# Kernel tuning notes

Hardware: AMD Instinct MI355X
Metric: run time of the kernel (lower is better)

## Reference

```python
import jax, jax.numpy as jnp
import numpy as np

VOCAB, EMBED, CONV_C, HID, LABELS = 50257, 512, 512, 1024, 128
B, S = 32, 1024

def setup_inputs() -> dict:
    key = jax.random.key(0)
    ks = jax.random.split(key, 8)
    sc = lambda d: 1.0 / np.sqrt(d)
    return {
        "token_ids": jax.random.randint(ks[0], (B, S), 0, VOCAB),
        "emb_table": jax.random.normal(ks[1], (VOCAB, EMBED), jnp.float32) * 0.02,
        "conv_w": jax.random.normal(ks[2], (CONV_C, EMBED), jnp.float32) * sc(EMBED),
        "conv_b": jnp.zeros((CONV_C,), jnp.float32),
        "dec_w1": jax.random.normal(ks[3], (CONV_C, HID), jnp.float32) * sc(CONV_C),
        "dec_b1": jnp.zeros((HID,), jnp.float32),
        "dec_w2": jax.random.normal(ks[4], (HID, LABELS), jnp.float32) * sc(HID),
        "dec_b2": jnp.zeros((LABELS,), jnp.float32),
    }

def reference(token_ids, emb_table, conv_w, conv_b, dec_w1, dec_b1, dec_w2, dec_b2):
    # Embedding lookup: [B, S, E]
    x = emb_table[token_ids]
    # DocNN encoder on a length-1 sequence = kernel-1 conv + relu (+ trivial max-over-time)
    h = jax.nn.relu(jnp.einsum('bse,ce->bsc', x, conv_w) + conv_b)  # [B,S,C]
    # MLP decoder per word
    z = jax.nn.relu(jnp.einsum('bsc,ch->bsh', h, dec_w1) + dec_b1)  # [B,S,H]
    logits = jnp.einsum('bsh,hl->bsl', z, dec_w2) + dec_b2          # [B,S,L]
    # torch.cat over dim 0 of per-word outputs -> flat [B*S, L]
    return logits.reshape(-1, logits.shape[-1])
```

## Files before the change

kernel.cpp:

```cpp
#include <hip/hip_runtime.h>

typedef __bf16 bf16;
typedef __bf16 bf16x4 __attribute__((ext_vector_type(4)));
typedef __bf16 bf16x8 __attribute__((ext_vector_type(8)));
typedef float f32x4 __attribute__((ext_vector_type(4)));

#define NROWS 32768
#define EMBED 512
#define CONV_C 512
#define HID 1024
#define LABELS 128

__device__ inline void async16(const void* g, void* l) {
  __builtin_amdgcn_global_load_lds(
      (const __attribute__((address_space(1))) void*)g,
      (__attribute__((address_space(3))) void*)l, 16, 0, 0);
}

__device__ inline bf16x8 cvt8_sw(const float* row, int o0, int o1) {
  f32x4 lo = *(const f32x4*)(row + o0);
  f32x4 hi = *(const f32x4*)(row + o1);
  bf16x8 r;
  r[0] = (bf16)lo[0]; r[1] = (bf16)lo[1]; r[2] = (bf16)lo[2]; r[3] = (bf16)lo[3];
  r[4] = (bf16)hi[0]; r[5] = (bf16)hi[1]; r[6] = (bf16)hi[2]; r[7] = (bf16)hi[3];
  return r;
}


__global__ void cvt_bf16(const float* __restrict__ in, bf16* __restrict__ out, int n) {
  int i = (blockIdx.x * blockDim.x + threadIdx.x) * 4;
  if (i >= n) return;
  float4 v = *(const float4*)(in + i);
  bf16x4 o;
  o.x = (bf16)v.x; o.y = (bf16)v.y; o.z = (bf16)v.z; o.w = (bf16)v.w;
  *(bf16x4*)(out + i) = o;
}

__global__ void transpose_cvt(const float* __restrict__ in, bf16* __restrict__ out,
                              int K, int N) {
  __shared__ float t[64][65];
  int kb = blockIdx.x * 64, nb = blockIdx.y * 64;
  for (int i = threadIdx.x; i < 4096; i += 256) {
    int r = i >> 6, c = i & 63;
    t[r][c] = in[(size_t)(kb + r) * N + nb + c];
  }
  __syncthreads();
  for (int i = threadIdx.x; i < 4096; i += 256) {
    int r = i >> 6, c = i & 63;
    out[(size_t)(nb + r) * K + kb + c] = (bf16)t[c][r];
  }
}

__global__ __launch_bounds__(256) void gemm1_gather(
    const int* __restrict__ tok, const float* __restrict__ emb,
    const bf16* __restrict__ convw, const float* __restrict__ bias,
    bf16* __restrict__ out, int M, int N, int K) {
  __shared__ __attribute__((aligned(16))) float lAf[128 * 32];
  __shared__ __attribute__((aligned(16))) bf16 lB[128 * 32];
  const int tid = threadIdx.x;
  const int wave = tid >> 6, lane = tid & 63;
  const int id = blockIdx.x;
  const int xcd = id & 7, q = id >> 3;
  const int nb = q & 3, mb = (q >> 2) * 8 + xcd;
  const int m0 = mb * 128, n0 = nb * 128;
  const int wm = (wave & 1) * 64, wn = (wave >> 1) * 64;
  const int lrow = lane & 15, quad = lane >> 4;
  const int slot0 = wave * 64 + lane;

  int arow[4], acol[4];
#pragma unroll
  for (int c = 0; c < 4; ++c) {
    int s = slot0 + c * 256;
    int r = s >> 3, p = s & 7;
    arow[c] = r;
    acol[c] = (p ^ (r & 7)) * 4;
  }
  int trow[4];
#pragma unroll
  for (int c = 0; c < 4; ++c) trow[c] = tok[m0 + arow[c]];

  const f32x4 zero4 = {0.f, 0.f, 0.f, 0.f};
  f32x4 acc[4][4];
#pragma unroll
  for (int i = 0; i < 4; ++i)
#pragma unroll
    for (int j = 0; j < 4; ++j) acc[i][j] = zero4;

  for (int k0 = 0; k0 < K; k0 += 32) {
#pragma unroll
    for (int c = 0; c < 4; ++c)
      async16(emb + (size_t)trow[c] * EMBED + k0 + acol[c],
              lAf + (size_t)(wave * 64 + c * 256) * 4);
#pragma unroll
    for (int c = 0; c < 2; ++c) {
      int s = slot0 + c * 256;
      int r = s >> 2, cs = s & 3;
      async16(convw + (size_t)(n0 + r) * K + k0 + cs * 8,
              lB + (size_t)(wave * 64 + c * 256) * 8);
    }
    __syncthreads();

    bf16x8 a[4], b[4];
#pragma unroll
    for (int t = 0; t < 4; ++t) {
      int r = wm + t * 16 + lrow, sw = r & 7;
      a[t] = cvt8_sw(lAf + r * 32, ((2 * quad) ^ sw) * 4, ((2 * quad + 1) ^ sw) * 4);
      b[t] = *(const bf16x8*)(lB + (wn + t * 16 + lrow) * 32 + quad * 8);
    }
#pragma unroll
    for (int mi = 0; mi < 4; ++mi)
#pragma unroll
      for (int ni = 0; ni < 4; ++ni)
        acc[mi][ni] =
            __builtin_amdgcn_mfma_f32_16x16x32_bf16(a[mi], b[ni], acc[mi][ni], 0, 0, 0);
    __syncthreads();
  }

#pragma unroll
  for (int mi = 0; mi < 4; ++mi) {
#pragma unroll
    for (int ni = 0; ni < 4; ++ni) {
      int col = n0 + wn + ni * 16 + lrow;
      float bv = bias[col];
#pragma unroll
      for (int r = 0; r < 4; ++r) {
        int row = m0 + wm + mi * 16 + quad * 4 + r;
        float v = acc[mi][ni][r] + bv;
        v = v > 0.f ? v : 0.f;
        out[(size_t)row * N + col] = (bf16)v;
      }
    }
  }
}

__global__ __launch_bounds__(256) void gemm23_fused(
    const bf16* __restrict__ h,
    const bf16* __restrict__ w1t,
    const bf16* __restrict__ w2t,
    const float* __restrict__ b1, const float* __restrict__ b2,
    float* __restrict__ out) {
  __shared__ __attribute__((aligned(16))) bf16 lA[64 * 32];
  __shared__ __attribute__((aligned(16))) bf16 lB[128 * 32];
  __shared__ __attribute__((aligned(16))) bf16 zbuf[64 * 128];
  __shared__ __attribute__((aligned(16))) bf16 lB3[128 * 128];
  const int tid = threadIdx.x, wave = tid >> 6, lane = tid & 63;
  const int m0 = blockIdx.x * 64;
  const int wm = (wave & 1) * 32, wn = (wave >> 1) * 64;
  const int lrow = lane & 15, quad = lane >> 4;
  const int slot0 = wave * 64 + lane;

  const f32x4 zero4 = {0.f, 0.f, 0.f, 0.f};
  f32x4 out_acc[2][4];
#pragma unroll
  for (int i = 0; i < 2; ++i)
#pragma unroll
    for (int j = 0; j < 4; ++j) out_acc[i][j] = zero4;

  for (int chunk = 0; chunk < 8; ++chunk) {
    f32x4 z_acc[2][4];
#pragma unroll
    for (int i = 0; i < 2; ++i)
#pragma unroll
      for (int j = 0; j < 4; ++j) z_acc[i][j] = zero4;

    const bf16* wB = w1t + (size_t)(chunk * 128) * 512;
    for (int k0 = 0; k0 < 512; k0 += 32) {
      {
        int r = slot0 >> 2, cs = slot0 & 3;
        async16(h + (size_t)(m0 + r) * 512 + k0 + cs * 8,
                lA + (size_t)(wave * 64) * 8);
      }
#pragma unroll
      for (int c = 0; c < 2; ++c) {
        int g = slot0 + c * 256;
        int r = g >> 2, cs = g & 3;
        async16(wB + (size_t)r * 512 + k0 + cs * 8,
                lB + (size_t)(wave * 64 + c * 256) * 8);
      }
      __syncthreads();

      bf16x8 a[2], b[4];
#pragma unroll
      for (int t = 0; t < 2; ++t)
        a[t] = *(const bf16x8*)(lA + (wm + t * 16 + lrow) * 32 + quad * 8);
#pragma unroll
      for (int t = 0; t < 4; ++t)
        b[t] = *(const bf16x8*)(lB + (wn + t * 16 + lrow) * 32 + quad * 8);
#pragma unroll
      for (int mi = 0; mi < 2; ++mi)
#pragma unroll
        for (int ni = 0; ni < 4; ++ni)
          z_acc[mi][ni] =
              __builtin_amdgcn_mfma_f32_16x16x32_bf16(a[mi], b[ni], z_acc[mi][ni], 0, 0, 0);
      __syncthreads();
    }

#pragma unroll
    for (int c = 0; c < 8; ++c) {
      int s = slot0 + c * 256;
      int r = s >> 4, p = s & 15;
      int qs = p ^ (r & 7);
      async16(w2t + (size_t)r * HID + chunk * 128 + qs * 8,
              lB3 + (size_t)(wave * 64 + c * 256) * 8);
    }
#pragma unroll
    for (int mi = 0; mi < 2; ++mi) {
#pragma unroll
      for (int ni = 0; ni < 4; ++ni) {
        int col = wn + ni * 16 + lrow;
        float bv = b1[chunk * 128 + col];
#pragma unroll
        for (int r = 0; r < 4; ++r) {
          int row = wm + mi * 16 + quad * 4 + r;
          float v = z_acc[mi][ni][r] + bv;
          v = v > 0.f ? v : 0.f;
          int g = col >> 3, wd = col & 7;
          int pos = g ^ (row & 7);
          zbuf[row * 128 + pos * 8 + wd] = (bf16)v;
        }
      }
    }
    __syncthreads();

#pragma unroll
    for (int ks = 0; ks < 4; ++ks) {
      bf16x8 a3[2], b3[4];
#pragma unroll
      for (int mi = 0; mi < 2; ++mi) {
        int row = wm + mi * 16 + lrow;
        int p = (ks * 4 + quad) ^ (row & 7);
        a3[mi] = *(const bf16x8*)(zbuf + row * 128 + p * 8);
      }
#pragma unroll
      for (int ni = 0; ni < 4; ++ni) {
        int row = wn + ni * 16 + lrow;
        int p = (ks * 4 + quad) ^ (row & 7);
        b3[ni] = *(const bf16x8*)(lB3 + row * 128 + p * 8);
      }
#pragma unroll
      for (int mi = 0; mi < 2; ++mi)
#pragma unroll
        for (int ni = 0; ni < 4; ++ni)
          out_acc[mi][ni] =
              __builtin_amdgcn_mfma_f32_16x16x32_bf16(a3[mi], b3[ni], out_acc[mi][ni], 0, 0, 0);
    }
    __syncthreads();
  }

#pragma unroll
  for (int mi = 0; mi < 2; ++mi) {
#pragma unroll
    for (int ni = 0; ni < 4; ++ni) {
      int col = wn + ni * 16 + lrow;
      float bv = b2[col];
#pragma unroll
      for (int r = 0; r < 4; ++r) {
        int row = m0 + wm + mi * 16 + quad * 4 + r;
        out[(size_t)row * LABELS + col] = out_acc[mi][ni][r] + bv;
      }
    }
  }
}


extern "C" void kernel_launch(void* const* d_in, const int* in_sizes, int n_in,
                              void* d_out, int out_size, void* d_ws, size_t ws_size,
                              hipStream_t stream) {
  const int* tok = (const int*)d_in[0];
  const float* emb = (const float*)d_in[1];
  const float* conv_w = (const float*)d_in[2];
  const float* conv_b = (const float*)d_in[3];
  const float* w1 = (const float*)d_in[4];
  const float* b1 = (const float*)d_in[5];
  const float* w2 = (const float*)d_in[6];
  const float* b2 = (const float*)d_in[7];
  float* out = (float*)d_out;

  char* ws = (char*)d_ws;
  bf16* wtc = (bf16*)(ws);
  bf16* wt1 = (bf16*)(ws + (1u << 19));
  bf16* wt2 = (bf16*)(ws + 3 * (1u << 19));
  bf16* h = (bf16*)(ws + (2u << 20));

  hipLaunchKernelGGL(cvt_bf16, dim3(256), dim3(256), 0, stream,
                     conv_w, wtc, CONV_C * EMBED);
  hipLaunchKernelGGL(transpose_cvt, dim3(8, 16), dim3(256), 0, stream,
                     w1, wt1, CONV_C, HID);
  hipLaunchKernelGGL(transpose_cvt, dim3(16, 2), dim3(256), 0, stream,
                     w2, wt2, HID, LABELS);

  hipLaunchKernelGGL(gemm1_gather, dim3(1024), dim3(256),
                     0, stream, tok, emb, wtc, conv_b, h, NROWS, CONV_C, EMBED);
  hipLaunchKernelGGL(gemm23_fused, dim3(NROWS / 64), dim3(256),
                     0, stream, h, wt1, wt2, b1, b2, out);
}
```

Measured before the change: 289.1 us.

## Double K-step in fused MLP GEMM, swizzle LDS layouts, simplify gemm1 grid

The fused decoder kernel now stages 64-wide K tiles instead of 32, which halves the number of barrier pairs per chunk. Its A/B tiles, zbuf and the W2 tile use new XOR swizzles, with the swizzle terms precomputed per thread, to avoid LDS bank conflicts. gemm1 drops its XCD-aware block remapping for a plain 2D grid. The cost is more shared memory per block and possibly worse L2 locality for gemm1 across XCDs.

```diff
diff --git a/kernel.cpp b/kernel.cpp
--- a/kernel.cpp
+++ b/kernel.cpp
@@ -15,6 +15,11 @@
   __builtin_amdgcn_global_load_lds(
       (const __attribute__((address_space(1))) void*)g,
       (__attribute__((address_space(3))) void*)l, 16, 0, 0);
+}
+
+__device__ inline int swap4(int x) { return ((x >> 2) | ((x & 3) << 2)) & 15; }
+__device__ inline int bitswap02(int g) {
+  return ((g & 1) << 2) | (g & 0xA) | ((g >> 2) & 1);
 }
 
 __device__ inline bf16x8 cvt8_sw(const float* row, int o0, int o1) {
@@ -59,10 +64,7 @@
   __shared__ __attribute__((aligned(16))) bf16 lB[128 * 32];
   const int tid = threadIdx.x;
   const int wave = tid >> 6, lane = tid & 63;
-  const int id = blockIdx.x;
-  const int xcd = id & 7, q = id >> 3;
-  const int nb = q & 3, mb = (q >> 2) * 8 + xcd;
-  const int m0 = mb * 128, n0 = nb * 128;
+  const int m0 = blockIdx.x * 128, n0 = blockIdx.y * 128;
   const int wm = (wave & 1) * 64, wn = (wave >> 1) * 64;
   const int lrow = lane & 15, quad = lane >> 4;
   const int slot0 = wave * 64 + lane;
@@ -139,8 +141,8 @@
     const bf16* __restrict__ w2t,
     const float* __restrict__ b1, const float* __restrict__ b2,
     float* __restrict__ out) {
-  __shared__ __attribute__((aligned(16))) bf16 lA[64 * 32];
-  __shared__ __attribute__((aligned(16))) bf16 lB[128 * 32];
+  __shared__ __attribute__((aligned(16))) bf16 lA[64 * 64];
+  __shared__ __attribute__((aligned(16))) bf16 lB[128 * 64];
   __shared__ __attribute__((aligned(16))) bf16 zbuf[64 * 128];
   __shared__ __attribute__((aligned(16))) bf16 lB3[128 * 128];
   const int tid = threadIdx.x, wave = tid >> 6, lane = tid & 63;
@@ -148,6 +150,29 @@
   const int wm = (wave & 1) * 32, wn = (wave >> 1) * 64;
   const int lrow = lane & 15, quad = lane >> 4;
   const int slot0 = wave * 64 + lane;
+  const int sw_lrow = swap4(lrow);
+
+  int a_r[2], a_c[2];
+#pragma unroll
+  for (int c = 0; c < 2; ++c) {
+    int s = slot0 + c * 256;
+    a_r[c] = s >> 3;
+    a_c[c] = ((s & 7) ^ (a_r[c] & 7)) * 8;
+  }
+  int b_r[4], b_c[4];
+#pragma unroll
+  for (int c = 0; c < 4; ++c) {
+    int s = slot0 + c * 256;
+    b_r[c] = s >> 3;
+    b_c[c] = ((s & 7) ^ (b_r[c] & 7)) * 8;
+  }
+  int w2_r[8], w2_c[8];
+#pragma unroll
+  for (int c = 0; c < 8; ++c) {
+    int s = slot0 + c * 256;
+    w2_r[c] = s >> 4;
+    w2_c[c] = bitswap02((s & 15) ^ swap4(w2_r[c] & 15)) * 8;
+  }
 
   const f32x4 zero4 = {0.f, 0.f, 0.f, 0.f};
   f32x4 out_acc[2][4];
@@ -164,59 +189,61 @@
       for (int j = 0; j < 4; ++j) z_acc[i][j] = zero4;
 
     const bf16* wB = w1t + (size_t)(chunk * 128) * 512;
-    for (int k0 = 0; k0 < 512; k0 += 32) {
-      {
-        int r = slot0 >> 2, cs = slot0 & 3;
-        async16(h + (size_t)(m0 + r) * 512 + k0 + cs * 8,
-                lA + (size_t)(wave * 64) * 8);
-      }
-#pragma unroll
-      for (int c = 0; c < 2; ++c) {
-        int g = slot0 + c * 256;
-        int r = g >> 2, cs = g & 3;
-        async16(wB + (size_t)r * 512 + k0 + cs * 8,
+    for (int k0 = 0; k0 < 512; k0 += 64) {
+#pragma unroll
+      for (int c = 0; c < 2; ++c)
+        async16(h + (size_t)(m0 + a_r[c]) * 512 + k0 + a_c[c],
+                lA + (size_t)(wave * 64 + c * 256) * 8);
+#pragma unroll
+      for (int c = 0; c < 4; ++c)
+        async16(wB + (size_t)b_r[c] * 512 + k0 + b_c[c],
                 lB + (size_t)(wave * 64 + c * 256) * 8);
-      }
       __syncthreads();
 
-      bf16x8 a[2], b[4];
-#pragma unroll
-      for (int t = 0; t < 2; ++t)
-        a[t] = *(const bf16x8*)(lA + (wm + t * 16 + lrow) * 32 + quad * 8);
-#pragma unroll
-      for (int t = 0; t < 4; ++t)
-        b[t] = *(const bf16x8*)(lB + (wn + t * 16 + lrow) * 32 + quad * 8);
-#pragma unroll
-      for (int mi = 0; mi < 2; ++mi)
-#pragma unroll
-        for (int ni = 0; ni < 4; ++ni)
-          z_acc[mi][ni] =
-              __builtin_amdgcn_mfma_f32_16x16x32_bf16(a[mi], b[ni], z_acc[mi][ni], 0, 0, 0);
+#pragma unroll
+      for (int ks = 0; ks < 2; ++ks) {
+        bf16x8 a[2], b[4];
+#pragma unroll
+        for (int t = 0; t < 2; ++t) {
+          int row = wm + t * 16 + lrow;
+          int pos = (ks * 4 + quad) ^ (row & 7);
+          a[t] = *(const bf16x8*)(lA + row * 64 + pos * 8);
+        }
+#pragma unroll
+        for (int t = 0; t < 4; ++t) {
+          int row = wn + t * 16 + lrow;
+          int pos = (ks * 4 + quad) ^ (row & 7);
+          b[t] = *(const bf16x8*)(lB + row * 64 + pos * 8);
+        }
+#pragma unroll
+        for (int mi = 0; mi < 2; ++mi)
+#pragma unroll
+          for (int ni = 0; ni < 4; ++ni)
+            z_acc[mi][ni] =
+                __builtin_amdgcn_mfma_f32_16x16x32_bf16(a[mi], b[ni], z_acc[mi][ni], 0, 0, 0);
+      }
       __syncthreads();
     }
 
 #pragma unroll
-    for (int c = 0; c < 8; ++c) {
-      int s = slot0 + c * 256;
-      int r = s >> 4, p = s & 15;
-      int qs = p ^ (r & 7);
-      async16(w2t + (size_t)r * HID + chunk * 128 + qs * 8,
+    for (int c = 0; c < 8; ++c)
+      async16(w2t + (size_t)w2_r[c] * HID + chunk * 128 + w2_c[c],
               lB3 + (size_t)(wave * 64 + c * 256) * 8);
-    }
+
 #pragma unroll
     for (int mi = 0; mi < 2; ++mi) {
 #pragma unroll
       for (int ni = 0; ni < 4; ++ni) {
         int col = wn + ni * 16 + lrow;
         float bv = b1[chunk * 128 + col];
+        int gsw = bitswap02(col >> 3);
 #pragma unroll
         for (int r = 0; r < 4; ++r) {
           int row = wm + mi * 16 + quad * 4 + r;
           float v = z_acc[mi][ni][r] + bv;
           v = v > 0.f ? v : 0.f;
-          int g = col >> 3, wd = col & 7;
-          int pos = g ^ (row & 7);
-          zbuf[row * 128 + pos * 8 + wd] = (bf16)v;
+          int pos = gsw ^ (quad | (r << 2));
+          zbuf[row * 128 + pos * 8 + (col & 7)] = (bf16)v;
         }
       }
     }
@@ -224,18 +251,17 @@
 
 #pragma unroll
     for (int ks = 0; ks < 4; ++ks) {
+      int possw = bitswap02(ks * 4 + quad) ^ sw_lrow;
       bf16x8 a3[2], b3[4];
 #pragma unroll
       for (int mi = 0; mi < 2; ++mi) {
         int row = wm + mi * 16 + lrow;
-        int p = (ks * 4 + quad) ^ (row & 7);
-        a3[mi] = *(const bf16x8*)(zbuf + row * 128 + p * 8);
+        a3[mi] = *(const bf16x8*)(zbuf + row * 128 + possw * 8);
       }
 #pragma unroll
       for (int ni = 0; ni < 4; ++ni) {
         int row = wn + ni * 16 + lrow;
-        int p = (ks * 4 + quad) ^ (row & 7);
-        b3[ni] = *(const bf16x8*)(lB3 + row * 128 + p * 8);
+        b3[ni] = *(const bf16x8*)(lB3 + row * 128 + possw * 8);
       }
 #pragma unroll
       for (int mi = 0; mi < 2; ++mi)
@@ -289,7 +315,7 @@
   hipLaunchKernelGGL(transpose_cvt, dim3(16, 2), dim3(256), 0, stream,
                      w2, wt2, HID, LABELS);
 
-  hipLaunchKernelGGL(gemm1_gather, dim3(1024), dim3(256),
+  hipLaunchKernelGGL(gemm1_gather, dim3(NROWS / 128, CONV_C / 128), dim3(256),
                      0, stream, tok, emb, wtc, conv_b, h, NROWS, CONV_C, EMBED);
   hipLaunchKernelGGL(gemm23_fused, dim3(NROWS / 64), dim3(256),
                      0, stream, h, wt1, wt2, b1, b2, out);
```

Measured after the change: 261.5 us. 1.11x faster.

## Load GEMM operands directly into registers with double buffering instead of LDS staging

Applied to the files above, without the earlier changes.

Both GEMM kernels drop LDS staging through global_load_lds and the per-k-step __syncthreads. Each wave now loads its A and B fragments straight from global memory into registers, with two-stage software double buffering. The second kernel also loads the w2 tile into registers and uses a new zbuf swizzle, and both kernels add a min-blocks-per-CU hint while gemm1 drops its XCD-aware block remap. This removes barrier stalls and LDS traffic, at the cost of redundant global and cache reads across waves, uncoalesced per-lane row loads, and higher register pressure.

```diff
diff --git a/kernel.cpp b/kernel.cpp
--- a/kernel.cpp
+++ b/kernel.cpp
@@ -11,15 +11,12 @@
 #define HID 1024
 #define LABELS 128
 
-__device__ inline void async16(const void* g, void* l) {
-  __builtin_amdgcn_global_load_lds(
-      (const __attribute__((address_space(1))) void*)g,
-      (__attribute__((address_space(3))) void*)l, 16, 0, 0);
-}
-
-__device__ inline bf16x8 cvt8_sw(const float* row, int o0, int o1) {
-  f32x4 lo = *(const f32x4*)(row + o0);
-  f32x4 hi = *(const f32x4*)(row + o1);
+__device__ inline int swap4(int x) { return ((x >> 2) | ((x & 3) << 2)) & 15; }
+__device__ inline int bitswap02(int g) {
+  return ((g & 1) << 2) | (g & 0xA) | ((g >> 2) & 1);
+}
+
+__device__ inline bf16x8 cvt8r(f32x4 lo, f32x4 hi) {
   bf16x8 r;
   r[0] = (bf16)lo[0]; r[1] = (bf16)lo[1]; r[2] = (bf16)lo[2]; r[3] = (bf16)lo[3];
   r[4] = (bf16)hi[0]; r[5] = (bf16)hi[1]; r[6] = (bf16)hi[2]; r[7] = (bf16)hi[3];
@@ -51,33 +48,23 @@
   }
 }
 
-__global__ __launch_bounds__(256) void gemm1_gather(
+__global__ __launch_bounds__(256, 2) void gemm1_reg(
     const int* __restrict__ tok, const float* __restrict__ emb,
     const bf16* __restrict__ convw, const float* __restrict__ bias,
-    bf16* __restrict__ out, int M, int N, int K) {
-  __shared__ __attribute__((aligned(16))) float lAf[128 * 32];
-  __shared__ __attribute__((aligned(16))) bf16 lB[128 * 32];
-  const int tid = threadIdx.x;
-  const int wave = tid >> 6, lane = tid & 63;
-  const int id = blockIdx.x;
-  const int xcd = id & 7, q = id >> 3;
-  const int nb = q & 3, mb = (q >> 2) * 8 + xcd;
-  const int m0 = mb * 128, n0 = nb * 128;
+    bf16* __restrict__ out) {
+  const int tid = threadIdx.x, wave = tid >> 6, lane = tid & 63;
+  const int m0 = blockIdx.x * 128, n0 = blockIdx.y * 128;
   const int wm = (wave & 1) * 64, wn = (wave >> 1) * 64;
   const int lrow = lane & 15, quad = lane >> 4;
-  const int slot0 = wave * 64 + lane;
-
-  int arow[4], acol[4];
-#pragma unroll
-  for (int c = 0; c < 4; ++c) {
-    int s = slot0 + c * 256;
-    int r = s >> 3, p = s & 7;
-    arow[c] = r;
-    acol[c] = (p ^ (r & 7)) * 4;
-  }
-  int trow[4];
-#pragma unroll
-  for (int c = 0; c < 4; ++c) trow[c] = tok[m0 + arow[c]];
+
+  const float* aptr[4];
+  const bf16* bptr[4];
+#pragma unroll
+  for (int t = 0; t < 4; ++t) {
+    int trow = tok[m0 + wm + t * 16 + lrow];
+    aptr[t] = emb + (size_t)trow * EMBED + quad * 8;
+    bptr[t] = convw + (size_t)(n0 + wn + t * 16 + lrow) * EMBED + quad * 8;
+  }
 
   const f32x4 zero4 = {0.f, 0.f, 0.f, 0.f};
   f32x4 acc[4][4];
@@ -86,35 +73,38 @@
 #pragma unroll
     for (int j = 0; j < 4; ++j) acc[i][j] = zero4;
 
-  for (int k0 = 0; k0 < K; k0 += 32) {
-#pragma unroll
-    for (int c = 0; c < 4; ++c)
-      async16(emb + (size_t)trow[c] * EMBED + k0 + acol[c],
-              lAf + (size_t)(wave * 64 + c * 256) * 4);
-#pragma unroll
-    for (int c = 0; c < 2; ++c) {
-      int s = slot0 + c * 256;
-      int r = s >> 2, cs = s & 3;
-      async16(convw + (size_t)(n0 + r) * K + k0 + cs * 8,
-              lB + (size_t)(wave * 64 + c * 256) * 8);
-    }
-    __syncthreads();
-
-    bf16x8 a[4], b[4];
-#pragma unroll
-    for (int t = 0; t < 4; ++t) {
-      int r = wm + t * 16 + lrow, sw = r & 7;
-      a[t] = cvt8_sw(lAf + r * 32, ((2 * quad) ^ sw) * 4, ((2 * quad + 1) ^ sw) * 4);
-      b[t] = *(const bf16x8*)(lB + (wn + t * 16 + lrow) * 32 + quad * 8);
-    }
-#pragma unroll
-    for (int mi = 0; mi < 4; ++mi)
-#pragma unroll
-      for (int ni = 0; ni < 4; ++ni)
-        acc[mi][ni] =
-            __builtin_amdgcn_mfma_f32_16x16x32_bf16(a[mi], b[ni], acc[mi][ni], 0, 0, 0);
-    __syncthreads();
-  }
+  f32x4 alo0[4], ahi0[4], alo1[4], ahi1[4];
+  bf16x8 b0[4], b1[4];
+
+#define LD1(alo, ahi, bb, k)                                   \
+  {                                                            \
+    _Pragma("unroll") for (int t = 0; t < 4; ++t) {            \
+      alo[t] = *(const f32x4*)(aptr[t] + (k));                 \
+      ahi[t] = *(const f32x4*)(aptr[t] + (k) + 4);             \
+      bb[t] = *(const bf16x8*)(bptr[t] + (k));                 \
+    }                                                          \
+  }
+#define STEP1(alo, ahi, bb)                                    \
+  {                                                            \
+    bf16x8 a[4];                                               \
+    _Pragma("unroll") for (int t = 0; t < 4; ++t)              \
+        a[t] = cvt8r(alo[t], ahi[t]);                          \
+    _Pragma("unroll") for (int mi = 0; mi < 4; ++mi)           \
+        _Pragma("unroll") for (int ni = 0; ni < 4; ++ni)       \
+            acc[mi][ni] = __builtin_amdgcn_mfma_f32_16x16x32_bf16( \
+                a[mi], bb[ni], acc[mi][ni], 0, 0, 0);          \
+  }
+
+  LD1(alo0, ahi0, b0, 0);
+#pragma unroll
+  for (int kk = 0; kk < 8; ++kk) {
+    LD1(alo1, ahi1, b1, kk * 64 + 32);
+    STEP1(alo0, ahi0, b0);
+    if (kk < 7) LD1(alo0, ahi0, b0, kk * 64 + 64);
+    STEP1(alo1, ahi1, b1);
+  }
+#undef LD1
+#undef STEP1
 
 #pragma unroll
   for (int mi = 0; mi < 4; ++mi) {
@@ -127,27 +117,33 @@
         int row = m0 + wm + mi * 16 + quad * 4 + r;
         float v = acc[mi][ni][r] + bv;
         v = v > 0.f ? v : 0.f;
-        out[(size_t)row * N + col] = (bf16)v;
-      }
-    }
-  }
-}
-
-__global__ __launch_bounds__(256) void gemm23_fused(
+        out[(size_t)row * CONV_C + col] = (bf16)v;
+      }
+    }
+  }
+}
+
+__global__ __launch_bounds__(256, 2) void gemm23_reg(
     const bf16* __restrict__ h,
     const bf16* __restrict__ w1t,
     const bf16* __restrict__ w2t,
     const float* __restrict__ b1, const float* __restrict__ b2,
     float* __restrict__ out) {
-  __shared__ __attribute__((aligned(16))) bf16 lA[64 * 32];
-  __shared__ __attribute__((aligned(16))) bf16 lB[128 * 32];
   __shared__ __attribute__((aligned(16))) bf16 zbuf[64 * 128];
-  __shared__ __attribute__((aligned(16))) bf16 lB3[128 * 128];
   const int tid = threadIdx.x, wave = tid >> 6, lane = tid & 63;
   const int m0 = blockIdx.x * 64;
   const int wm = (wave & 1) * 32, wn = (wave >> 1) * 64;
   const int lrow = lane & 15, quad = lane >> 4;
-  const int slot0 = wave * 64 + lane;
+  const int sw_lrow = swap4(lrow);
+
+  const bf16* aptr[2];
+#pragma unroll
+  for (int t = 0; t < 2; ++t)
+    aptr[t] = h + (size_t)(m0 + wm + t * 16 + lrow) * 512 + quad * 8;
+  const bf16* b3ptr[4];
+#pragma unroll
+  for (int t = 0; t < 4; ++t)
+    b3ptr[t] = w2t + (size_t)(wn + t * 16 + lrow) * HID + quad * 8;
 
   const f32x4 zero4 = {0.f, 0.f, 0.f, 0.f};
   f32x4 out_acc[2][4];
@@ -157,94 +153,85 @@
     for (int j = 0; j < 4; ++j) out_acc[i][j] = zero4;
 
   for (int chunk = 0; chunk < 8; ++chunk) {
+    const bf16* bptr[4];
+#pragma unroll
+    for (int t = 0; t < 4; ++t)
+      bptr[t] = w1t + (size_t)(chunk * 128 + wn + t * 16 + lrow) * 512 + quad * 8;
+
     f32x4 z_acc[2][4];
 #pragma unroll
     for (int i = 0; i < 2; ++i)
 #pragma unroll
       for (int j = 0; j < 4; ++j) z_acc[i][j] = zero4;
 
-    const bf16* wB = w1t + (size_t)(chunk * 128) * 512;
-    for (int k0 = 0; k0 < 512; k0 += 32) {
-      {
-        int r = slot0 >> 2, cs = slot0 & 3;
-        async16(h + (size_t)(m0 + r) * 512 + k0 + cs * 8,
-                lA + (size_t)(wave * 64) * 8);
-      }
-#pragma unroll
-      for (int c = 0; c < 2; ++c) {
-        int g = slot0 + c * 256;
-        int r = g >> 2, cs = g & 3;
-        async16(wB + (size_t)r * 512 + k0 + cs * 8,
-                lB + (size_t)(wave * 64 + c * 256) * 8);
-      }
-      __syncthreads();
-
-      bf16x8 a[2], b[4];
-#pragma unroll
-      for (int t = 0; t < 2; ++t)
-        a[t] = *(const bf16x8*)(lA + (wm + t * 16 + lrow) * 32 + quad * 8);
-#pragma unroll
-      for (int t = 0; t < 4; ++t)
-        b[t] = *(const bf16x8*)(lB + (wn + t * 16 + lrow) * 32 + quad * 8);
-#pragma unroll
-      for (int mi = 0; mi < 2; ++mi)
-#pragma unroll
-        for (int ni = 0; ni < 4; ++ni)
-          z_acc[mi][ni] =
-              __builtin_amdgcn_mfma_f32_16x16x32_bf16(a[mi], b[ni], z_acc[mi][ni], 0, 0, 0);
-      __syncthreads();
-    }
-
-#pragma unroll
-    for (int c = 0; c < 8; ++c) {
-      int s = slot0 + c * 256;
-      int r = s >> 4, p = s & 15;
-      int qs = p ^ (r & 7);
-      async16(w2t + (size_t)r * HID + chunk * 128 + qs * 8,
-              lB3 + (size_t)(wave * 64 + c * 256) * 8);
-    }
+    bf16x8 a0[2], a1[2], b0[4], b1v[4];
+#define LD2(aa, bb, k)                                         \
+  {                                                            \
+    _Pragma("unroll") for (int t = 0; t < 2; ++t)              \
+        aa[t] = *(const bf16x8*)(aptr[t] + (k));               \
+    _Pragma("unroll") for (int t = 0; t < 4; ++t)              \
+        bb[t] = *(const bf16x8*)(bptr[t] + (k));               \
+  }
+#define STEP2(aa, bb)                                          \
+  {                                                            \
+    _Pragma("unroll") for (int mi = 0; mi < 2; ++mi)           \
+        _Pragma("unroll") for (int ni = 0; ni < 4; ++ni)       \
+            z_acc[mi][ni] = __builtin_amdgcn_mfma_f32_16x16x32_bf16( \
+                aa[mi], bb[ni], z_acc[mi][ni], 0, 0, 0);       \
+  }
+    LD2(a0, b0, 0);
+#pragma unroll
+    for (int kk = 0; kk < 8; ++kk) {
+      LD2(a1, b1v, kk * 64 + 32);
+      STEP2(a0, b0);
+      if (kk < 7) LD2(a0, b0, kk * 64 + 64);
+      STEP2(a1, b1v);
+    }
+#undef LD2
+#undef STEP2
+
+    __syncthreads();
 #pragma unroll
     for (int mi = 0; mi < 2; ++mi) {
 #pragma unroll
       for (int ni = 0; ni < 4; ++ni) {
         int col = wn + ni * 16 + lrow;
         float bv = b1[chunk * 128 + col];
+        int gsw = bitswap02(col >> 3);
 #pragma unroll
         for (int r = 0; r < 4; ++r) {
           int row = wm + mi * 16 + quad * 4 + r;
           float v = z_acc[mi][ni][r] + bv;
           v = v > 0.f ? v : 0.f;
-          int g = col >> 3, wd = col & 7;
-          int pos = g ^ (row & 7);
-          zbuf[row * 128 + pos * 8 + wd] = (bf16)v;
+          int pos = gsw ^ (quad | (r << 2));
+          zbuf[row * 128 + pos * 8 + (col & 7)] = (bf16)v;
         }
       }
     }
+    bf16x8 b3[4][4];
+#pragma unroll
+    for (int ni = 0; ni < 4; ++ni)
+#pragma unroll
+      for (int ks = 0; ks < 4; ++ks)
+        b3[ni][ks] = *(const bf16x8*)(b3ptr[ni] + chunk * 128 + ks * 32);
     __syncthreads();
 
 #pragma unroll
     for (int ks = 0; ks < 4; ++ks) {
-      bf16x8 a3[2], b3[4];
+      int possw = bitswap02(ks * 4 + quad) ^ sw_lrow;
+      bf16x8 a3[2];
 #pragma unroll
       for (int mi = 0; mi < 2; ++mi) {
         int row = wm + mi * 16 + lrow;
-        int p = (ks * 4 + quad) ^ (row & 7);
-        a3[mi] = *(const bf16x8*)(zbuf + row * 128 + p * 8);
-      }
-#pragma unroll
-      for (int ni = 0; ni < 4; ++ni) {
-        int row = wn + ni * 16 + lrow;
-        int p = (ks * 4 + quad) ^ (row & 7);
-        b3[ni] = *(const bf16x8*)(lB3 + row * 128 + p * 8);
+        a3[mi] = *(const bf16x8*)(zbuf + row * 128 + possw * 8);
       }
 #pragma unroll
       for (int mi = 0; mi < 2; ++mi)
 #pragma unroll
         for (int ni = 0; ni < 4; ++ni)
-          out_acc[mi][ni] =
-              __builtin_amdgcn_mfma_f32_16x16x32_bf16(a3[mi], b3[ni], out_acc[mi][ni], 0, 0, 0);
-    }
-    __syncthreads();
+          out_acc[mi][ni] = __builtin_amdgcn_mfma_f32_16x16x32_bf16(
+              a3[mi], b3[ni][ks], out_acc[mi][ni], 0, 0, 0);
+    }
   }
 
 #pragma unroll
@@ -289,8 +276,8 @@
   hipLaunchKernelGGL(transpose_cvt, dim3(16, 2), dim3(256), 0, stream,
                      w2, wt2, HID, LABELS);
 
-  hipLaunchKernelGGL(gemm1_gather, dim3(1024), dim3(256),
-                     0, stream, tok, emb, wtc, conv_b, h, NROWS, CONV_C, EMBED);
-  hipLaunchKernelGGL(gemm23_fused, dim3(NROWS / 64), dim3(256),
+  hipLaunchKernelGGL(gemm1_reg, dim3(NROWS / 128, CONV_C / 128), dim3(256),
+                     0, stream, tok, emb, wtc, conv_b, h);
+  hipLaunchKernelGGL(gemm23_reg, dim3(NROWS / 64), dim3(256),
                      0, stream, h, wt1, wt2, b1, b2, out);
 }
```

Result: slower. 442.6 us (+53.1%).
